# Optimization experiments

Hardware: AMD Instinct MI355X
Metric: run time of the kernel (lower is better)

## Reference

```python
import jax, jax.numpy as jnp
import numpy as np

B, F, T = 32, 512, 2048


def setup_inputs() -> dict:
    key = jax.random.key(0)
    k1, k2 = jax.random.split(key)
    predicted = jax.random.uniform(k1, (B, F, T), dtype=jnp.float32)
    gt = jax.random.randint(k2, (B, F, T), 0, 2, dtype=jnp.int32)
    return {"predicted": predicted, "gt": gt}


def reference(predicted, gt):
    # The 3x3 kernel has only its center set to 1. Tracing every branch of the
    # original per-point loop shows each GT peak (b, f, t) contributes exactly
    # one element of `predicted`:
    #   row f' = f+1 if f == 0 else f   (edge slicing shifts the pick at f==0)
    #   col t' = t+1 if t == 0 else t   (same at t==0)
    # Vectorize by remapping row 0 -> row 1 and col 0 -> col 1 once, then doing
    # a masked sum over all GT-nonzero positions.
    Fdim, Tdim = predicted.shape[1], predicted.shape[2]
    ridx = jnp.where(jnp.arange(Fdim) == 0, 1, jnp.arange(Fdim))
    cidx = jnp.where(jnp.arange(Tdim) == 0, 1, jnp.arange(Tdim))
    p_adj = predicted[:, ridx][:, :, cidx]          # [B, F, T]
    mask = (gt != 0).astype(predicted.dtype)        # [B, F, T]
    count = jnp.sum(mask)
    retrieved = jnp.sum(p_adj * mask)
    # Original returns 0.0 when there are no GT peaks.
    return jnp.where(count > 0, retrieved / count, jnp.zeros((), predicted.dtype))
```

## Files before the change

kernel.cpp:

```cpp
#include <hip/hip_runtime.h>
#include <stdint.h>


constexpr int B_ = 32;
constexpr int F_ = 512;
constexpr int T_ = 2048;
constexpr long long NTOT = (long long)B_ * F_ * T_;
constexpr int NQ      = (int)(NTOT >> 2);
constexpr int BLK     = 256;
constexpr int NBLK    = 4096;
constexpr int PER_THR = 8;
static_assert((long long)BLK * NBLK * PER_THR == NQ, "exact cover");

constexpr int EDGE_ITEMS = B_ * T_ + B_ * F_;
constexpr int EDGE_BLKS  = EDGE_ITEMS / BLK;

typedef float vf4 __attribute__((ext_vector_type(4)));
typedef int   vi4 __attribute__((ext_vector_type(4)));

__device__ __forceinline__ void block_reduce(float& s, int& c) {
    #pragma unroll
    for (int off = 32; off > 0; off >>= 1) {
        s += __shfl_down(s, off, 64);
        c += __shfl_down(c, off, 64);
    }
    __shared__ float ss[4];
    __shared__ int   sc[4];
    int lane = threadIdx.x & 63, wave = threadIdx.x >> 6;
    if (lane == 0) { ss[wave] = s; sc[wave] = c; }
    __syncthreads();
    if (threadIdx.x == 0) {
        s = ss[0] + ss[1] + ss[2] + ss[3];
        c = sc[0] + sc[1] + sc[2] + sc[3];
    }
}

__global__ __launch_bounds__(256, 1) void recall_main(
    const float* __restrict__ pred,
    const int* __restrict__ gt,
    float* __restrict__ bsum,
    unsigned int* __restrict__ bcnt)
{
    const unsigned tid    = blockIdx.x * BLK + threadIdx.x;
    const unsigned STRIDE = (unsigned)BLK * NBLK;

    vf4 p[PER_THR];
    vi4 g[PER_THR];

    #pragma unroll
    for (int k = 0; k < PER_THR; ++k) {
        uint64_t pa = (uint64_t)(pred) + ((uint64_t)tid + (uint64_t)k * STRIDE) * 16u;
        uint64_t ga = (uint64_t)(gt)   + ((uint64_t)tid + (uint64_t)k * STRIDE) * 16u;
        asm volatile("global_load_dwordx4 %0, %1, off" : "=v"(p[k]) : "v"(pa));
        asm volatile("global_load_dwordx4 %0, %1, off" : "=v"(g[k]) : "v"(ga));
    }

    float lsum = 0.f;
    int   lcnt = 0;
    #pragma unroll
    for (int k = 0; k < PER_THR; ++k) {
        asm volatile("s_waitcnt vmcnt(%2)"
                     : "+v"(p[k]), "+v"(g[k])
                     : "n"(14 - 2 * k));
        lcnt += (g[k].x != 0) + (g[k].y != 0) + (g[k].z != 0) + (g[k].w != 0);
        lsum += (g[k].x ? p[k].x : 0.f);
        lsum += (g[k].y ? p[k].y : 0.f);
        lsum += (g[k].z ? p[k].z : 0.f);
        lsum += (g[k].w ? p[k].w : 0.f);
    }

    block_reduce(lsum, lcnt);
    if (threadIdx.x == 0) {
        bsum[blockIdx.x] = lsum;
        bcnt[blockIdx.x] = (unsigned int)lcnt;
    }
}

__global__ __launch_bounds__(256) void recall_edge(
    const float* __restrict__ pred,
    const int* __restrict__ gt,
    float* __restrict__ csum)
{
    unsigned idx = blockIdx.x * BLK + threadIdx.x;
    float corr = 0.f;
    if (idx < (unsigned)(B_ * T_)) {
        unsigned b = idx >> 11, t = idx & (T_ - 1);
        unsigned raw = (b << 20) | t;
        unsigned tp  = (t == 0u) ? 1u : t;
        unsigned adj = (b << 20) | (1u << 11) | tp;
        if (gt[raw]) corr = pred[adj] - pred[raw];
    } else {
        unsigned i2 = idx - (unsigned)(B_ * T_);
        unsigned b = i2 >> 9, f = i2 & (F_ - 1);
        if (f != 0u) {
            unsigned raw = (b << 20) | (f << 11);
            if (gt[raw]) corr = pred[raw + 1] - pred[raw];
        }
    }
    int dummy = 0;
    block_reduce(corr, dummy);
    if (threadIdx.x == 0) csum[blockIdx.x] = corr;
}

__global__ __launch_bounds__(256) void recall_fin(
    const float* __restrict__ bsum,
    const unsigned int* __restrict__ bcnt,
    const float* __restrict__ csum,
    float* __restrict__ out)
{
    float s = 0.f;
    int   c = 0;
    for (int j = threadIdx.x; j < NBLK; j += BLK) {
        s += bsum[j];
        c += (int)bcnt[j];
    }
    for (int j = threadIdx.x; j < EDGE_BLKS; j += BLK) s += csum[j];

    block_reduce(s, c);
    if (threadIdx.x == 0)
        out[0] = (c > 0) ? (s / (float)c) : 0.0f;
}

extern "C" void kernel_launch(void* const* d_in, const int* in_sizes, int n_in,
                              void* d_out, int out_size, void* d_ws, size_t ws_size,
                              hipStream_t stream)
{
    const float* pred = (const float*)d_in[0];
    const int*   gt   = (const int*)d_in[1];
    float*       out  = (float*)d_out;

    float*        bsum = (float*)d_ws;
    unsigned int* bcnt = (unsigned int*)((char*)d_ws + NBLK * sizeof(float));
    float*        csum = (float*)((char*)d_ws + 2 * NBLK * sizeof(float));

    recall_main<<<NBLK, BLK, 0, stream>>>(pred, gt, bsum, bcnt);
    recall_edge<<<EDGE_BLKS, BLK, 0, stream>>>(pred, gt, csum);
    recall_fin<<<1, BLK, 0, stream>>>(bsum, bcnt, csum, out);
}
```

Measured before the change: 295.6 us.

## Stage main reduction through LDS using direct global-to-LDS loads

Replaces the register-resident strided dwordx4 loads in the main reduction kernel with global_load_lds transfers into shared memory. The kernel now runs 1024 blocks, each looping over 8 contiguous chunks of 4096 elements, synchronizing before and after reading the chunk from LDS. This aims to cut register pressure and improve load streaming. In exchange it adds two block barriers per iteration and loses overlap between loading and compute, because the chunks are not double-buffered.

```diff
diff --git a/kernel.cpp b/kernel.cpp
--- a/kernel.cpp
+++ b/kernel.cpp
@@ -6,17 +6,17 @@
 constexpr int F_ = 512;
 constexpr int T_ = 2048;
 constexpr long long NTOT = (long long)B_ * F_ * T_;
-constexpr int NQ      = (int)(NTOT >> 2);
-constexpr int BLK     = 256;
-constexpr int NBLK    = 4096;
-constexpr int PER_THR = 8;
-static_assert((long long)BLK * NBLK * PER_THR == NQ, "exact cover");
+constexpr int BLK   = 256;
+constexpr int NBLK  = 1024;
+constexpr int CHUNK = 4096;
+constexpr int ITERS = 8;
+static_assert((long long)NBLK * CHUNK * ITERS == NTOT, "exact cover");
 
 constexpr int EDGE_ITEMS = B_ * T_ + B_ * F_;
 constexpr int EDGE_BLKS  = EDGE_ITEMS / BLK;
 
-typedef float vf4 __attribute__((ext_vector_type(4)));
-typedef int   vi4 __attribute__((ext_vector_type(4)));
+typedef const __attribute__((address_space(1))) void* gvp;
+typedef __attribute__((address_space(3))) void* lvp;
 
 __device__ __forceinline__ void block_reduce(float& s, int& c) {
     #pragma unroll
@@ -35,38 +35,49 @@
     }
 }
 
-__global__ __launch_bounds__(256, 1) void recall_main(
+__global__ __launch_bounds__(256) void recall_main(
     const float* __restrict__ pred,
     const int* __restrict__ gt,
     float* __restrict__ bsum,
     unsigned int* __restrict__ bcnt)
 {
-    const unsigned tid    = blockIdx.x * BLK + threadIdx.x;
-    const unsigned STRIDE = (unsigned)BLK * NBLK;
+    __shared__ float ps[CHUNK];
+    __shared__ int   gs[CHUNK];
 
-    vf4 p[PER_THR];
-    vi4 g[PER_THR];
-
-    #pragma unroll
-    for (int k = 0; k < PER_THR; ++k) {
-        uint64_t pa = (uint64_t)(pred) + ((uint64_t)tid + (uint64_t)k * STRIDE) * 16u;
-        uint64_t ga = (uint64_t)(gt)   + ((uint64_t)tid + (uint64_t)k * STRIDE) * 16u;
-        asm volatile("global_load_dwordx4 %0, %1, off" : "=v"(p[k]) : "v"(pa));
-        asm volatile("global_load_dwordx4 %0, %1, off" : "=v"(g[k]) : "v"(ga));
-    }
+    const int t    = threadIdx.x;
+    const int lane = t & 63;
+    const int wave = t >> 6;
+    const size_t block_base = (size_t)blockIdx.x * ((size_t)CHUNK * ITERS);
 
     float lsum = 0.f;
     int   lcnt = 0;
-    #pragma unroll
-    for (int k = 0; k < PER_THR; ++k) {
-        asm volatile("s_waitcnt vmcnt(%2)"
-                     : "+v"(p[k]), "+v"(g[k])
-                     : "n"(14 - 2 * k));
-        lcnt += (g[k].x != 0) + (g[k].y != 0) + (g[k].z != 0) + (g[k].w != 0);
-        lsum += (g[k].x ? p[k].x : 0.f);
-        lsum += (g[k].y ? p[k].y : 0.f);
-        lsum += (g[k].z ? p[k].z : 0.f);
-        lsum += (g[k].w ? p[k].w : 0.f);
+
+    for (int it = 0; it < ITERS; ++it) {
+        const size_t chunk = block_base + (size_t)it * CHUNK;
+
+        #pragma unroll
+        for (int k = 0; k < 4; ++k) {
+            size_t e = chunk + (size_t)wave * 1024 + (size_t)k * 256 + (size_t)lane * 4;
+            __builtin_amdgcn_global_load_lds(
+                (gvp)(pred + e), (lvp)(&ps[wave * 1024 + k * 256]), 16, 0, 0);
+            __builtin_amdgcn_global_load_lds(
+                (gvp)(gt + e),   (lvp)(&gs[wave * 1024 + k * 256]), 16, 0, 0);
+        }
+        __syncthreads();
+
+        const float4* p4 = (const float4*)ps;
+        const int4*   g4 = (const int4*)gs;
+        #pragma unroll
+        for (int j = 0; j < 4; ++j) {
+            float4 p = p4[t + j * 256];
+            int4   g = g4[t + j * 256];
+            lcnt += (g.x != 0) + (g.y != 0) + (g.z != 0) + (g.w != 0);
+            lsum += (g.x ? p.x : 0.f);
+            lsum += (g.y ? p.y : 0.f);
+            lsum += (g.z ? p.z : 0.f);
+            lsum += (g.w ? p.w : 0.f);
+        }
+        __syncthreads();
     }
 
     block_reduce(lsum, lcnt);
```

New measurement: 284.2 us. -3.8%, faster.
